# Optimization experiments

Hardware: AMD Instinct MI355X
Metric: run time of the kernel (lower is better)

Reference implementation:

```python
import jax, jax.numpy as jnp
import numpy as np

HEADS = 8
DIM_HEAD = 160
QUERY_DIM = 1280
INNER = HEADS * DIM_HEAD  # 1280
B, S = 2, 4096


def setup_inputs() -> dict:
    key = jax.random.key(0)
    ks = jax.random.split(key, 7)
    scale = 0.02
    return {
        "hidden_states": jax.random.normal(ks[0], (B, QUERY_DIM, 1, S), jnp.float32),
        "context": jax.random.normal(ks[1], (B, QUERY_DIM, 1, S), jnp.float32),
        "mask": jnp.zeros((B, S, 1, 1), jnp.float32),
        "Wq": jax.random.normal(ks[2], (INNER, QUERY_DIM), jnp.float32) * scale,
        "Wk": jax.random.normal(ks[3], (INNER, QUERY_DIM), jnp.float32) * scale,
        "Wv": jax.random.normal(ks[4], (INNER, QUERY_DIM), jnp.float32) * scale,
        "Wout": jax.random.normal(ks[5], (QUERY_DIM, INNER), jnp.float32) * scale,
        "bout": jnp.zeros((QUERY_DIM,), jnp.float32),
    }


def reference(hidden_states, context, mask, Wq, Wk, Wv, Wout, bout):
    # hidden_states/context: [B, C, 1, S]; 1x1 conv == channel-dim matmul.
    x = hidden_states[:, :, 0, :]  # [B, C, Sq]
    c = context[:, :, 0, :]        # [B, C, Sk]
    scale = DIM_HEAD ** (-0.5)

    q = jnp.einsum("oc,bcs->bos", Wq, x)  # [B, inner, Sq]
    k = jnp.einsum("oc,bcs->bos", Wk, c)  # [B, inner, Sk]
    v = jnp.einsum("oc,bcs->bos", Wv, c)  # [B, inner, Sk]

    bsz, _, sq = q.shape
    sk = k.shape[-1]
    qh = q.reshape(bsz, HEADS, DIM_HEAD, sq)
    kh = k.reshape(bsz, HEADS, DIM_HEAD, sk)
    vh = v.reshape(bsz, HEADS, DIM_HEAD, sk)

    # split_einsum: per-head q^T k * scale, mask added per kv position,
    # softmax over kv dim. Vectorized over heads here (same math).
    scores = jnp.einsum("bhdq,bhdk->bhqk", qh, kh) * scale  # [B,H,Sq,Sk]
    scores = scores + mask[:, 0:, 0, 0][:, None, None, :]   # mask over kv
    weights = jax.nn.softmax(scores, axis=-1)
    attn = jnp.einsum("bhqk,bhdk->bhdq", weights, vh)       # [B,H,Dh,Sq]
    attn = attn.reshape(bsz, INNER, sq)

    out = jnp.einsum("oc,bcs->bos", Wout, attn) + bout[None, :, None]
    return out[:, :, None, :]  # [B, C, 1, Sq]
```

## Files before the change

### kernel.cpp

```cpp
#include <hip/hip_runtime.h>
#include <hip/hip_bf16.h>
#include <math.h>

#define B_   2
#define S_   4096
#define H_   8
#define D_   160
#define QD_  1280
#define SCALE 0.07905694150420949f
#define LOG2E 1.4426950408889634f

typedef unsigned short ushort_t;
typedef __attribute__((ext_vector_type(8))) short short8;
typedef __attribute__((ext_vector_type(4))) float f32x4;

#define MFMA16(a, b, c) __builtin_amdgcn_mfma_f32_16x16x32_bf16(a, b, c, 0, 0, 0)

__device__ __forceinline__ ushort_t f2bf(float f) {
  unsigned u = __float_as_uint(f);
  u += 0x7fffu + ((u >> 16) & 1u);
  return (ushort_t)(u >> 16);
}
__device__ __forceinline__ ushort_t f2bf_fast(float f) {
  return (ushort_t)((__float_as_uint(f) + 0x8000u) >> 16);
}

__device__ __forceinline__ void gload_lds16(const ushort_t* g, ushort_t* l) {
  __builtin_amdgcn_global_load_lds(
      (const __attribute__((address_space(1))) unsigned int*)(g),
      (__attribute__((address_space(3))) unsigned int*)(l), 16, 0, 0);
}

template <int CTRL>
__device__ __forceinline__ float dpp_mov(float x) {
  return __int_as_float(
      __builtin_amdgcn_update_dpp(0, __float_as_int(x), CTRL, 0xF, 0xF, true));
}
__device__ __forceinline__ float row_sum16(float x) {
  x += dpp_mov<0xB1>(x);
  x += dpp_mov<0x4E>(x);
  x += dpp_mov<0x124>(x);
  x += dpp_mov<0x128>(x);
  return x;
}

__global__ __launch_bounds__(256) void transpose_cvt2(
    const float* __restrict__ xs, const float* __restrict__ cs,
    ushort_t* __restrict__ Xt, ushort_t* __restrict__ Ct)
{
  const int z = blockIdx.z;
  const int b = z & 1;
  const float* src = (z < 2) ? xs : cs;
  ushort_t* dst    = (z < 2) ? Xt : Ct;
  const int s0 = blockIdx.x * 32;
  const int c0 = blockIdx.y * 32;
  __shared__ float T[32][33];
  const int t = threadIdx.x;
  const int sl = t & 31, cr = t >> 5;
#pragma unroll
  for (int i = 0; i < 4; ++i)
    T[cr + i * 8][sl] = src[((size_t)b * QD_ + c0 + cr + i * 8) * S_ + s0 + sl];
  __syncthreads();
  const int cl = (t & 7) * 4, sr = t >> 3;
  ushort4 v;
  v.x = f2bf(T[cl + 0][sr]);
  v.y = f2bf(T[cl + 1][sr]);
  v.z = f2bf(T[cl + 2][sr]);
  v.w = f2bf(T[cl + 3][sr]);
  *(ushort4*)(dst + ((size_t)b * S_ + s0 + sr) * QD_ + c0 + cl) = v;
}

__global__ __launch_bounds__(256) void cvt_w(
    const float* __restrict__ w0, const float* __restrict__ w1,
    const float* __restrict__ w2, const float* __restrict__ w3,
    ushort_t* __restrict__ o0, ushort_t* __restrict__ o1,
    ushort_t* __restrict__ o2, ushort_t* __restrict__ o3)
{
  const int which = blockIdx.y;
  const float* s = which == 0 ? w0 : which == 1 ? w1 : which == 2 ? w2 : w3;
  ushort_t* d    = which == 0 ? o0 : which == 1 ? o1 : which == 2 ? o2 : o3;
  const size_t i = ((size_t)blockIdx.x * 256 + threadIdx.x) * 4;
  const float4 f = *(const float4*)(s + i);
  ushort4 v;
  v.x = f2bf(f.x); v.y = f2bf(f.y); v.z = f2bf(f.z); v.w = f2bf(f.w);
  *(ushort4*)(d + i) = v;
}

#define QBM 256
#define QBN 256
#define QBK 32

#define QKV_STAGE(tt, p)                                                       \
  {                                                                            \
    const int k0s = (tt) * QBK;                                                \
    _Pragma("unroll")                                                          \
    for (int i = 0; i < 2; ++i) {                                              \
      const int G = (i * 8 + wid) * 64 + lane;                                 \
      const int r = G >> 2, sl = G & 3;                                        \
      const int g = sl ^ (r & 3);                                              \
      gload_lds16(Ab + (size_t)(m0 + r) * QD_ + k0s + g * 8,                   \
                  &As[p][(size_t)(i * 8 + wid) * 512]);                        \
      gload_lds16(Bb + (size_t)(n0 + r) * QD_ + k0s + g * 8,                   \
                  &Bs[p][(size_t)(i * 8 + wid) * 512]);                        \
    }                                                                          \
  }

__global__ __launch_bounds__(512) void gemm_qkv(
    const ushort_t* __restrict__ Xt, const ushort_t* __restrict__ Ct,
    const ushort_t* __restrict__ Wqb, const ushort_t* __restrict__ Wkb,
    const ushort_t* __restrict__ Wvb,
    ushort_t* __restrict__ q_ws, ushort_t* __restrict__ k_ws,
    ushort_t* __restrict__ v_ws)
{
  const size_t PB = (size_t)S_ * QD_;
  const int which = blockIdx.z >> 1, b = blockIdx.z & 1;
  const ushort_t* Ab;
  const ushort_t* Bb;
  ushort_t* Cb;
  int Nv, nxb, cm, cn;
  if (which == 0) {
    Ab = Xt + (size_t)b * PB; Bb = Wqb; Cb = q_ws + (size_t)b * PB;
    Nv = QD_; nxb = 5; cm = 2; cn = 5;
  } else if (which == 1) {
    Ab = Ct + (size_t)b * PB; Bb = Wkb; Cb = k_ws + (size_t)b * PB;
    Nv = QD_; nxb = 5; cm = 2; cn = 5;
  } else {
    Ab = Wvb; Bb = Ct + (size_t)b * PB; Cb = v_ws + (size_t)b * PB;
    Nv = S_; nxb = 16; cm = 5; cn = 2;
  }
  const int tiles_x = nxb / cn;
  const int orig = blockIdx.x;
  const int xcd = orig & 7, idx = orig >> 3;
  const int trow = xcd / tiles_x, tcol = xcd - trow * tiles_x;
  const int m0 = (trow * cm + idx / cn) * QBM;
  const int n0 = (tcol * cn + idx % cn) * QBN;

  __shared__ ushort_t As[3][QBM * QBK];
  __shared__ ushort_t Bs[3][QBN * QBK];

  const int t = threadIdx.x;
  const int wid = t >> 6, lane = t & 63;
  const int l16 = lane & 15, quad = lane >> 4;
  const int wm = (wid >> 2) * 128, wn = (wid & 3) * 64;

  f32x4 acc[8][4];
#pragma unroll
  for (int i = 0; i < 8; ++i)
#pragma unroll
    for (int j = 0; j < 4; ++j) acc[i][j] = {0.f, 0.f, 0.f, 0.f};

  const int NIT = QD_ / QBK;
  QKV_STAGE(0, 0);
  QKV_STAGE(1, 1);
  for (int it = 0; it < NIT; ++it) {
    if (it + 1 < NIT) {
      asm volatile("s_waitcnt vmcnt(4)" ::: "memory");
    } else {
      asm volatile("s_waitcnt vmcnt(0)" ::: "memory");
    }
    __builtin_amdgcn_sched_barrier(0);
    __builtin_amdgcn_s_barrier();
    __builtin_amdgcn_sched_barrier(0);
    if (it + 2 < NIT) {
      QKV_STAGE(it + 2, (it + 2) % 3);
      __builtin_amdgcn_sched_barrier(0);
    }
    const int p = it % 3;
    short8 af[8], bfr[4];
#pragma unroll
    for (int mt = 0; mt < 8; ++mt) {
      const int r = wm + mt * 16 + l16;
      af[mt] = *(const short8*)&As[p][r * 32 + ((quad ^ (r & 3)) << 3)];
    }
#pragma unroll
    for (int nt = 0; nt < 4; ++nt) {
      const int r = wn + nt * 16 + l16;
      bfr[nt] = *(const short8*)&Bs[p][r * 32 + ((quad ^ (r & 3)) << 3)];
    }
#pragma unroll
    for (int mt = 0; mt < 8; ++mt)
#pragma unroll
      for (int nt = 0; nt < 4; ++nt)
        acc[mt][nt] = MFMA16(af[mt], bfr[nt], acc[mt][nt]);
  }

#pragma unroll
  for (int mt = 0; mt < 8; ++mt)
#pragma unroll
    for (int r = 0; r < 4; ++r) {
      const int row = m0 + wm + mt * 16 + quad * 4 + r;
      ushort_t* cr = Cb + (size_t)row * Nv + n0 + wn + l16;
#pragma unroll
      for (int nt = 0; nt < 4; ++nt) cr[nt * 16] = f2bf_fast(acc[mt][nt][r]);
    }
}

#define GBM 128
#define GBN 128
#define GBK 32

#define GEMM_STAGE(tt, p, Abp, Bbp, Kv)                                        \
  {                                                                            \
    const int k0s = (tt) * GBK;                                                \
    _Pragma("unroll")                                                          \
    for (int i = 0; i < 2; ++i) {                                              \
      const int G = (i * 4 + wid) * 64 + lane;                                 \
      const int r = G >> 2, sl = G & 3;                                        \
      const int g = sl ^ (r & 3);                                              \
      gload_lds16(Abp + (size_t)(m0 + r) * (Kv) + k0s + g * 8,                 \
                  &As[p][(i * 4 + wid) * 512]);                                \
      gload_lds16(Bbp + (size_t)(n0 + r) * (Kv) + k0s + g * 8,                 \
                  &Bs[p][(i * 4 + wid) * 512]);                                \
    }                                                                          \
  }

#define GEMM_PIPE_ITER(it, NIT, Abp, Bbp, Kv)                                  \
  {                                                                            \
    if ((it) + 1 < (NIT)) {                                                    \
      asm volatile("s_waitcnt vmcnt(4)" ::: "memory");                         \
    } else {                                                                   \
      asm volatile("s_waitcnt vmcnt(0)" ::: "memory");                         \
    }                                                                          \
    __builtin_amdgcn_sched_barrier(0);                                         \
    __builtin_amdgcn_s_barrier();                                              \
    __builtin_amdgcn_sched_barrier(0);                                         \
    if ((it) + 2 < (NIT)) {                                                    \
      GEMM_STAGE((it) + 2, ((it) + 2) % 3, Abp, Bbp, Kv);                      \
      __builtin_amdgcn_sched_barrier(0);                                       \
    }                                                                          \
    const int p = (it) % 3;                                                    \
    short8 af[4], bfr[4];                                                      \
    _Pragma("unroll")                                                          \
    for (int mt = 0; mt < 4; ++mt) {                                           \
      const int r = wm + mt * 16 + l16;                                        \
      af[mt] = *(const short8*)&As[p][r * 32 + ((quad ^ (r & 3)) << 3)];       \
    }                                                                          \
    _Pragma("unroll")                                                          \
    for (int nt = 0; nt < 4; ++nt) {                                           \
      const int r = wn + nt * 16 + l16;                                        \
      bfr[nt] = *(const short8*)&Bs[p][r * 32 + ((quad ^ (r & 3)) << 3)];      \
    }                                                                          \
    _Pragma("unroll")                                                          \
    for (int mt = 0; mt < 4; ++mt)                                             \
      _Pragma("unroll")                                                        \
      for (int nt = 0; nt < 4; ++nt)                                           \
        acc[mt][nt] = MFMA16(af[mt], bfr[nt], acc[mt][nt]);                    \
  }

__global__ __launch_bounds__(256) void gemm_mfma(
    const ushort_t* __restrict__ A, const ushort_t* __restrict__ B,
    void* __restrict__ Cp, const float* __restrict__ bias,
    int M, int N, int K, int mode,
    size_t strideA, size_t strideB, size_t strideC,
    int cm, int cn)
{
  const int bz = blockIdx.z;
  const int nx = gridDim.x;
  const int tiles_x = nx / cn;
  const int orig = blockIdx.x + nx * blockIdx.y;
  const int xcd = orig & 7;
  const int idx = orig >> 3;
  const int trow = xcd / tiles_x, tcol = xcd - trow * tiles_x;
  const int m0 = (trow * cm + idx / cn) * GBM;
  const int n0 = (tcol * cn + idx % cn) * GBN;

  const ushort_t* __restrict__ Ab = A + (size_t)bz * strideA;
  const ushort_t* __restrict__ Bb = B + (size_t)bz * strideB;

  __shared__ ushort_t As[3][GBM * GBK];
  __shared__ ushort_t Bs[3][GBN * GBK];

  const int t = threadIdx.x;
  const int wid = t >> 6, lane = t & 63;
  const int l16 = lane & 15, quad = lane >> 4;
  const int wm = (wid >> 1) * 64, wn = (wid & 1) * 64;

  f32x4 acc[4][4];
#pragma unroll
  for (int i = 0; i < 4; ++i)
#pragma unroll
    for (int j = 0; j < 4; ++j) acc[i][j] = {0.f, 0.f, 0.f, 0.f};

  const int NIT = K / GBK;
  GEMM_STAGE(0, 0, Ab, Bb, K);
  GEMM_STAGE(1, 1, Ab, Bb, K);
  for (int it = 0; it < NIT; ++it) {
    GEMM_PIPE_ITER(it, NIT, Ab, Bb, K);
  }

  if (mode == 0) {
    ushort_t* C = (ushort_t*)Cp + (size_t)bz * strideC;
#pragma unroll
    for (int mt = 0; mt < 4; ++mt)
#pragma unroll
      for (int r = 0; r < 4; ++r) {
        const int row = m0 + wm + mt * 16 + quad * 4 + r;
        ushort_t* cr = C + (size_t)row * N + n0 + wn + l16;
#pragma unroll
        for (int nt = 0; nt < 4; ++nt) cr[nt * 16] = f2bf_fast(acc[mt][nt][r]);
      }
  } else {
    float* C = (float*)Cp + (size_t)bz * strideC;
#pragma unroll
    for (int mt = 0; mt < 4; ++mt)
#pragma unroll
      for (int r = 0; r < 4; ++r) {
        const int row = m0 + wm + mt * 16 + quad * 4 + r;
        const float bv = bias[row];
        float* cr = C + (size_t)row * N + n0 + wn + l16;
#pragma unroll
        for (int nt = 0; nt < 4; ++nt) cr[nt * 16] = acc[mt][nt][r] + bv;
      }
  }
}

#define TQ 128
#define TK 64
#define KTSTR 168
#define VTSTR 72
#define PSTR  72

__global__ __launch_bounds__(256, 2) void flash_attn_mfma(
    const ushort_t* __restrict__ qws, const ushort_t* __restrict__ kws,
    const ushort_t* __restrict__ vws, const float* __restrict__ mask,
    ushort_t* __restrict__ attn_out)
{
  const int b  = blockIdx.z;
  const int orig = blockIdx.x + 32 * blockIdx.y;
  const int swz  = ((orig & 7) << 5) | (orig >> 3);
  const int q0 = (swz & 31) * TQ;
  const int h  = swz >> 5;
  const int t  = threadIdx.x;
  const int wid  = t >> 6;
  const int lane = t & 63;
  const int l16  = lane & 15;
  const int quad = lane >> 4;

  __shared__ __align__(16) ushort_t smem[31744];
  ushort_t* Kt = smem;
  ushort_t* Vt = smem + 1344 * 8;
  ushort_t* Pp = smem + 2816 * 8;

  int goff[11];
#pragma unroll
  for (int jj = 0; jj < 11; ++jj) {
    const int j = jj * 4 + wid;
    const int slot = j * 64 + lane;
    int off;
    if (j < 21) {
      const int r = slot / 21, c = slot - r * 21;
      off = (c < 20) ? r * QD_ + c * 8 : 0;
    } else {
      const int vs = slot - 1344;
      const int r = vs / 9, c = vs - r * 9;
      off = (c < 8 && r < 160) ? r * S_ + c * 8 : 0;
    }
    goff[jj] = off;
  }

  const ushort_t* kg = kws + (size_t)b * S_ * QD_ + h * D_;
  const ushort_t* vg = vws + ((size_t)b * QD_ + h * D_) * S_;

  short8 aq[2][5];
#pragma unroll
  for (int mt = 0; mt < 2; ++mt) {
    const ushort_t* qrow =
        qws + ((size_t)(b * S_ + q0 + wid * 32 + mt * 16 + l16)) * QD_ + h * D_;
#pragma unroll
    for (int dc = 0; dc < 5; ++dc)
      aq[mt][dc] = *(const short8*)(qrow + dc * 32 + quad * 8);
  }

#pragma unroll
  for (int jj = 0; jj < 6; ++jj) {
    const int j = jj * 4 + wid;
    if (j < 21) gload_lds16(kg + goff[jj], &smem[(size_t)j * 512]);
  }
#pragma unroll
  for (int jj = 5; jj < 11; ++jj) {
    const int j = jj * 4 + wid;
    if (j >= 21) gload_lds16(vg + goff[jj], &smem[(size_t)j * 512]);
  }

  f32x4 Oa[2][10];
#pragma unroll
  for (int mt = 0; mt < 2; ++mt)
#pragma unroll
    for (int nt = 0; nt < 10; ++nt) Oa[mt][nt] = {0.f, 0.f, 0.f, 0.f};
  float lpart[2][4] = {{0.f, 0.f, 0.f, 0.f}, {0.f, 0.f, 0.f, 0.f}};
  const float SC2 = SCALE * LOG2E;

  const int pswz = quad << 4;
  const int prsw = (l16 >> 2) << 4;

  for (int kp0 = 0; kp0 < S_; kp0 += TK) {
    asm volatile("s_waitcnt vmcnt(5)" ::: "memory");
    __builtin_amdgcn_sched_barrier(0);
    __builtin_amdgcn_s_barrier();
    __builtin_amdgcn_sched_barrier(0);

    float mv[4];
#pragma unroll
    for (int c = 0; c < 4; ++c)
      mv[c] = mask[b * S_ + kp0 + c * 16 + l16] * LOG2E;

    f32x4 s[2][4];
#pragma unroll
    for (int mt = 0; mt < 2; ++mt)
#pragma unroll
      for (int c = 0; c < 4; ++c) s[mt][c] = {0.f, 0.f, 0.f, 0.f};
    __builtin_amdgcn_s_setprio(1);
#pragma unroll
    for (int dc = 0; dc < 5; ++dc) {
      short8 bb[4];
#pragma unroll
      for (int c = 0; c < 4; ++c)
        bb[c] = *(const short8*)&Kt[(c * 16 + l16) * KTSTR + dc * 32 + quad * 8];
#pragma unroll
      for (int mt = 0; mt < 2; ++mt)
#pragma unroll
        for (int c = 0; c < 4; ++c)
          s[mt][c] = MFMA16(aq[mt][dc], bb[c], s[mt][c]);
    }
    __builtin_amdgcn_s_setprio(0);

    ushort_t* pw = Pp + wid * (32 * PSTR);
#pragma unroll
    for (int mt = 0; mt < 2; ++mt)
#pragma unroll
      for (int r = 0; r < 4; ++r) {
        const float p0 = exp2f(s[mt][0][r] * SC2 + mv[0]);
        const float p1 = exp2f(s[mt][1][r] * SC2 + mv[1]);
        const float p2 = exp2f(s[mt][2][r] * SC2 + mv[2]);
        const float p3 = exp2f(s[mt][3][r] * SC2 + mv[3]);
        lpart[mt][r] += (p0 + p1) + (p2 + p3);
        ushort_t* prow = pw + (mt * 16 + quad * 4 + r) * PSTR;
        prow[(pswz ^  0) + l16] = f2bf_fast(p0);
        prow[(pswz ^ 16) + l16] = f2bf_fast(p1);
        prow[(pswz ^ 32) + l16] = f2bf_fast(p2);
        prow[(pswz ^ 48) + l16] = f2bf_fast(p3);
      }

    short8 ap[2][2];
#pragma unroll
    for (int mt = 0; mt < 2; ++mt) {
#pragma unroll
      for (int ks = 0; ks < 2; ++ks)
        ap[mt][ks] = *(const short8*)
            &Pp[wid * (32 * PSTR) + (mt * 16 + l16) * PSTR +
                ((ks * 32 + quad * 8) ^ prsw)];
    }

    __syncthreads();

    const int kn = kp0 + TK;
    if (kn < S_) {
      const ushort_t* kgn = kg + (size_t)kn * QD_;
#pragma unroll
      for (int jj = 0; jj < 6; ++jj) {
        const int j = jj * 4 + wid;
        if (j < 21) gload_lds16(kgn + goff[jj], &smem[(size_t)j * 512]);
      }
      __builtin_amdgcn_sched_barrier(0);
    }

    __builtin_amdgcn_s_setprio(1);
#pragma unroll
    for (int nt = 0; nt < 10; ++nt) {
      const short8 bv0 = *(const short8*)&Vt[(nt * 16 + l16) * VTSTR + quad * 8];
      const short8 bv1 = *(const short8*)&Vt[(nt * 16 + l16) * VTSTR + 32 + quad * 8];
#pragma unroll
      for (int mt = 0; mt < 2; ++mt) {
        Oa[mt][nt] = MFMA16(ap[mt][0], bv0, Oa[mt][nt]);
        Oa[mt][nt] = MFMA16(ap[mt][1], bv1, Oa[mt][nt]);
      }
    }
    __builtin_amdgcn_s_setprio(0);

    __builtin_amdgcn_sched_barrier(0);
    __builtin_amdgcn_s_barrier();
    __builtin_amdgcn_sched_barrier(0);

    if (kn < S_) {
      const ushort_t* vgn = vg + kn;
#pragma unroll
      for (int jj = 5; jj < 11; ++jj) {
        const int j = jj * 4 + wid;
        if (j >= 21) gload_lds16(vgn + goff[jj], &smem[(size_t)j * 512]);
      }
    }
  }

#pragma unroll
  for (int mt = 0; mt < 2; ++mt)
#pragma unroll
    for (int r = 0; r < 4; ++r) {
      const float l = row_sum16(lpart[mt][r]);
      const float inv = 1.f / l;
      const int qq = q0 + wid * 32 + mt * 16 + quad * 4 + r;
      ushort_t* orow = attn_out + ((size_t)(b * S_ + qq)) * QD_ + h * D_;
#pragma unroll
      for (int nt = 0; nt < 10; ++nt)
        orow[nt * 16 + l16] = f2bf_fast(Oa[mt][nt][r] * inv);
    }
}

extern "C" void kernel_launch(void* const* d_in, const int* in_sizes, int n_in,
                              void* d_out, int out_size, void* d_ws, size_t ws_size,
                              hipStream_t stream) {
  const float* x    = (const float*)d_in[0];
  const float* c    = (const float*)d_in[1];
  const float* mask = (const float*)d_in[2];
  const float* Wq   = (const float*)d_in[3];
  const float* Wk   = (const float*)d_in[4];
  const float* Wv   = (const float*)d_in[5];
  const float* Wout = (const float*)d_in[6];
  const float* bout = (const float*)d_in[7];
  float* out = (float*)d_out;

  const size_t PB   = (size_t)S_ * QD_;
  const size_t NELT = (size_t)B_ * PB;
  const size_t WN   = (size_t)QD_ * QD_;

  ushort_t* Xt    = (ushort_t*)d_ws;
  ushort_t* Ct    = Xt + NELT;
  ushort_t* Wqb   = Ct + NELT;
  ushort_t* Wkb   = Wqb + WN;
  ushort_t* Wvb   = Wkb + WN;
  ushort_t* Woutb = Wvb + WN;
  ushort_t* q_ws  = Woutb + WN;
  ushort_t* k_ws  = q_ws + NELT;
  ushort_t* v_ws  = k_ws + NELT;
  ushort_t* attn_ws = v_ws + NELT;

  const dim3 tgrid(S_ / 32, QD_ / 32, 2 * B_);
  transpose_cvt2<<<tgrid, 256, 0, stream>>>(x, c, Xt, Ct);
  cvt_w<<<dim3(WN / 1024, 4, 1), 256, 0, stream>>>(Wq, Wk, Wv, Wout,
                                                   Wqb, Wkb, Wvb, Woutb);

  gemm_qkv<<<dim3(80, 1, 6), 512, 0, stream>>>(Xt, Ct, Wqb, Wkb, Wvb,
                                               q_ws, k_ws, v_ws);

  const dim3 agrid(S_ / TQ, H_, B_);
  flash_attn_mfma<<<agrid, 256, 0, stream>>>(q_ws, k_ws, v_ws, mask, attn_ws);

  const dim3 gv(S_ / GBN, QD_ / GBM, B_);
  gemm_mfma<<<gv, 256, 0, stream>>>(Woutb, attn_ws, out, bout,
                                    QD_, S_, QD_, 1, 0, PB, PB, 5, 8);
}
```

Before: 526.3 us.

## Split flash-attention block across 8 waves with 16 query rows each

The attention kernel now launches 512 threads per block instead of 256. Each of the 8 waves owns 16 query rows instead of 32, which halves per-wave accumulator and Q-fragment registers. The K/V tile-load work is redistributed across 8 waves and the vmcnt wait is lowered to match the fewer loads per wave. This aims for more waves in flight to hide latency, at the cost of less MFMA reuse of each K/V LDS fragment per wave and more barrier participants. The per-block LDS footprint is unchanged.

Result: slower. 608.2 us (+15.6%).

```diff
diff --git a/kernel.cpp b/kernel.cpp
--- a/kernel.cpp
+++ b/kernel.cpp
@@ -320,7 +320,7 @@
 #define VTSTR 72
 #define PSTR  72
 
-__global__ __launch_bounds__(256, 2) void flash_attn_mfma(
+__global__ __launch_bounds__(512, 4) void flash_attn_mfma(
     const ushort_t* __restrict__ qws, const ushort_t* __restrict__ kws,
     const ushort_t* __restrict__ vws, const float* __restrict__ mask,
     ushort_t* __restrict__ attn_out)
@@ -341,16 +341,16 @@
   ushort_t* Vt = smem + 1344 * 8;
   ushort_t* Pp = smem + 2816 * 8;
 
-  int goff[11];
-#pragma unroll
-  for (int jj = 0; jj < 11; ++jj) {
-    const int j = jj * 4 + wid;
+  int goff[6];
+#pragma unroll
+  for (int jj = 0; jj < 6; ++jj) {
+    const int j = jj * 8 + wid;
     const int slot = j * 64 + lane;
-    int off;
+    int off = 0;
     if (j < 21) {
       const int r = slot / 21, c = slot - r * 21;
       off = (c < 20) ? r * QD_ + c * 8 : 0;
-    } else {
+    } else if (j < 44) {
       const int vs = slot - 1344;
       const int r = vs / 9, c = vs - r * 9;
       off = (c < 8 && r < 160) ? r * S_ + c * 8 : 0;
@@ -361,40 +361,37 @@
   const ushort_t* kg = kws + (size_t)b * S_ * QD_ + h * D_;
   const ushort_t* vg = vws + ((size_t)b * QD_ + h * D_) * S_;
 
-  short8 aq[2][5];
-#pragma unroll
-  for (int mt = 0; mt < 2; ++mt) {
+  short8 aq[5];
+  {
     const ushort_t* qrow =
-        qws + ((size_t)(b * S_ + q0 + wid * 32 + mt * 16 + l16)) * QD_ + h * D_;
+        qws + ((size_t)(b * S_ + q0 + wid * 16 + l16)) * QD_ + h * D_;
 #pragma unroll
     for (int dc = 0; dc < 5; ++dc)
-      aq[mt][dc] = *(const short8*)(qrow + dc * 32 + quad * 8);
+      aq[dc] = *(const short8*)(qrow + dc * 32 + quad * 8);
   }
 
 #pragma unroll
   for (int jj = 0; jj < 6; ++jj) {
-    const int j = jj * 4 + wid;
+    const int j = jj * 8 + wid;
     if (j < 21) gload_lds16(kg + goff[jj], &smem[(size_t)j * 512]);
   }
 #pragma unroll
-  for (int jj = 5; jj < 11; ++jj) {
-    const int j = jj * 4 + wid;
-    if (j >= 21) gload_lds16(vg + goff[jj], &smem[(size_t)j * 512]);
-  }
-
-  f32x4 Oa[2][10];
-#pragma unroll
-  for (int mt = 0; mt < 2; ++mt)
-#pragma unroll
-    for (int nt = 0; nt < 10; ++nt) Oa[mt][nt] = {0.f, 0.f, 0.f, 0.f};
-  float lpart[2][4] = {{0.f, 0.f, 0.f, 0.f}, {0.f, 0.f, 0.f, 0.f}};
+  for (int jj = 0; jj < 6; ++jj) {
+    const int j = jj * 8 + wid;
+    if (j >= 21 && j < 44) gload_lds16(vg + goff[jj], &smem[(size_t)j * 512]);
+  }
+
+  f32x4 Oa[10];
+#pragma unroll
+  for (int nt = 0; nt < 10; ++nt) Oa[nt] = {0.f, 0.f, 0.f, 0.f};
+  float lpart[4] = {0.f, 0.f, 0.f, 0.f};
   const float SC2 = SCALE * LOG2E;
 
   const int pswz = quad << 4;
   const int prsw = (l16 >> 2) << 4;
 
   for (int kp0 = 0; kp0 < S_; kp0 += TK) {
-    asm volatile("s_waitcnt vmcnt(5)" ::: "memory");
+    asm volatile("s_waitcnt vmcnt(2)" ::: "memory");
     __builtin_amdgcn_sched_barrier(0);
     __builtin_amdgcn_s_barrier();
     __builtin_amdgcn_sched_barrier(0);
@@ -404,11 +401,9 @@
     for (int c = 0; c < 4; ++c)
       mv[c] = mask[b * S_ + kp0 + c * 16 + l16] * LOG2E;
 
-    f32x4 s[2][4];
-#pragma unroll
-    for (int mt = 0; mt < 2; ++mt)
-#pragma unroll
-      for (int c = 0; c < 4; ++c) s[mt][c] = {0.f, 0.f, 0.f, 0.f};
+    f32x4 s[4];
+#pragma unroll
+    for (int c = 0; c < 4; ++c) s[c] = {0.f, 0.f, 0.f, 0.f};
     __builtin_amdgcn_s_setprio(1);
 #pragma unroll
     for (int dc = 0; dc < 5; ++dc) {
@@ -417,39 +412,31 @@
       for (int c = 0; c < 4; ++c)
         bb[c] = *(const short8*)&Kt[(c * 16 + l16) * KTSTR + dc * 32 + quad * 8];
 #pragma unroll
-      for (int mt = 0; mt < 2; ++mt)
-#pragma unroll
-        for (int c = 0; c < 4; ++c)
-          s[mt][c] = MFMA16(aq[mt][dc], bb[c], s[mt][c]);
+      for (int c = 0; c < 4; ++c)
+        s[c] = MFMA16(aq[dc], bb[c], s[c]);
     }
     __builtin_amdgcn_s_setprio(0);
 
-    ushort_t* pw = Pp + wid * (32 * PSTR);
-#pragma unroll
-    for (int mt = 0; mt < 2; ++mt)
-#pragma unroll
-      for (int r = 0; r < 4; ++r) {
-        const float p0 = exp2f(s[mt][0][r] * SC2 + mv[0]);
-        const float p1 = exp2f(s[mt][1][r] * SC2 + mv[1]);
-        const float p2 = exp2f(s[mt][2][r] * SC2 + mv[2]);
-        const float p3 = exp2f(s[mt][3][r] * SC2 + mv[3]);
-        lpart[mt][r] += (p0 + p1) + (p2 + p3);
-        ushort_t* prow = pw + (mt * 16 + quad * 4 + r) * PSTR;
-        prow[(pswz ^  0) + l16] = f2bf_fast(p0);
-        prow[(pswz ^ 16) + l16] = f2bf_fast(p1);
-        prow[(pswz ^ 32) + l16] = f2bf_fast(p2);
-        prow[(pswz ^ 48) + l16] = f2bf_fast(p3);
-      }
-
-    short8 ap[2][2];
-#pragma unroll
-    for (int mt = 0; mt < 2; ++mt) {
-#pragma unroll
-      for (int ks = 0; ks < 2; ++ks)
-        ap[mt][ks] = *(const short8*)
-            &Pp[wid * (32 * PSTR) + (mt * 16 + l16) * PSTR +
-                ((ks * 32 + quad * 8) ^ prsw)];
-    }
+    ushort_t* pw = Pp + wid * (16 * PSTR);
+#pragma unroll
+    for (int r = 0; r < 4; ++r) {
+      const float p0 = exp2f(s[0][r] * SC2 + mv[0]);
+      const float p1 = exp2f(s[1][r] * SC2 + mv[1]);
+      const float p2 = exp2f(s[2][r] * SC2 + mv[2]);
+      const float p3 = exp2f(s[3][r] * SC2 + mv[3]);
+      lpart[r] += (p0 + p1) + (p2 + p3);
+      ushort_t* prow = pw + (quad * 4 + r) * PSTR;
+      prow[(pswz ^  0) + l16] = f2bf_fast(p0);
+      prow[(pswz ^ 16) + l16] = f2bf_fast(p1);
+      prow[(pswz ^ 32) + l16] = f2bf_fast(p2);
+      prow[(pswz ^ 48) + l16] = f2bf_fast(p3);
+    }
+
+    short8 ap[2];
+#pragma unroll
+    for (int ks = 0; ks < 2; ++ks)
+      ap[ks] = *(const short8*)
+          &Pp[wid * (16 * PSTR) + l16 * PSTR + ((ks * 32 + quad * 8) ^ prsw)];
 
     __syncthreads();
 
@@ -458,7 +445,7 @@
       const ushort_t* kgn = kg + (size_t)kn * QD_;
 #pragma unroll
       for (int jj = 0; jj < 6; ++jj) {
-        const int j = jj * 4 + wid;
+        const int j = jj * 8 + wid;
         if (j < 21) gload_lds16(kgn + goff[jj], &smem[(size_t)j * 512]);
       }
       __builtin_amdgcn_sched_barrier(0);
@@ -469,11 +456,8 @@
     for (int nt = 0; nt < 10; ++nt) {
       const short8 bv0 = *(const short8*)&Vt[(nt * 16 + l16) * VTSTR + quad * 8];
       const short8 bv1 = *(const short8*)&Vt[(nt * 16 + l16) * VTSTR + 32 + quad * 8];
-#pragma unroll
-      for (int mt = 0; mt < 2; ++mt) {
-        Oa[mt][nt] = MFMA16(ap[mt][0], bv0, Oa[mt][nt]);
-        Oa[mt][nt] = MFMA16(ap[mt][1], bv1, Oa[mt][nt]);
-      }
+      Oa[nt] = MFMA16(ap[0], bv0, Oa[nt]);
+      Oa[nt] = MFMA16(ap[1], bv1, Oa[nt]);
     }
     __builtin_amdgcn_s_setprio(0);
 
@@ -484,25 +468,23 @@
     if (kn < S_) {
       const ushort_t* vgn = vg + kn;
 #pragma unroll
-      for (int jj = 5; jj < 11; ++jj) {
-        const int j = jj * 4 + wid;
-        if (j >= 21) gload_lds16(vgn + goff[jj], &smem[(size_t)j * 512]);
+      for (int jj = 0; jj < 6; ++jj) {
+        const int j = jj * 8 + wid;
+        if (j >= 21 && j < 44) gload_lds16(vgn + goff[jj], &smem[(size_t)j * 512]);
       }
     }
   }
 
 #pragma unroll
-  for (int mt = 0; mt < 2; ++mt)
-#pragma unroll
-    for (int r = 0; r < 4; ++r) {
-      const float l = row_sum16(lpart[mt][r]);
-      const float inv = 1.f / l;
-      const int qq = q0 + wid * 32 + mt * 16 + quad * 4 + r;
-      ushort_t* orow = attn_out + ((size_t)(b * S_ + qq)) * QD_ + h * D_;
-#pragma unroll
-      for (int nt = 0; nt < 10; ++nt)
-        orow[nt * 16 + l16] = f2bf_fast(Oa[mt][nt][r] * inv);
-    }
+  for (int r = 0; r < 4; ++r) {
+    const float l = row_sum16(lpart[r]);
+    const float inv = 1.f / l;
+    const int qq = q0 + wid * 16 + quad * 4 + r;
+    ushort_t* orow = attn_out + ((size_t)(b * S_ + qq)) * QD_ + h * D_;
+#pragma unroll
+    for (int nt = 0; nt < 10; ++nt)
+      orow[nt * 16 + l16] = f2bf_fast(Oa[nt][r] * inv);
+  }
 }
 
 extern "C" void kernel_launch(void* const* d_in, const int* in_sizes, int n_in,
@@ -542,7 +524,7 @@
                                                q_ws, k_ws, v_ws);
 
   const dim3 agrid(S_ / TQ, H_, B_);
-  flash_attn_mfma<<<agrid, 256, 0, stream>>>(q_ws, k_ws, v_ws, mask, attn_ws);
+  flash_attn_mfma<<<agrid, 512, 0, stream>>>(q_ws, k_ws, v_ws, mask, attn_ws);
 
   const dim3 gv(S_ / GBN, QD_ / GBM, B_);
   gemm_mfma<<<gv, 256, 0, stream>>>(Woutb, attn_ws, out, bout,
```
